# Kernel optimization log

Measured on AMD Instinct MI355X. Metric: run time of the kernel, lower is better.

The kernel has to match this reference:

```python
import jax, jax.numpy as jnp
import numpy as np

C_IN = 1024
N_HEADS = 16
C_HEAD = C_IN // N_HEADS  # 64
ROPE_BASE = 10000.0


def setup_inputs() -> dict:
    key = jax.random.key(0)
    ks = jax.random.split(key, 7)
    B, S = 2, 2048
    q = jax.random.normal(ks[0], (B, S, C_IN), dtype=jnp.float32)
    k = jax.random.normal(ks[1], (B, S, C_IN), dtype=jnp.float32)
    v = jax.random.normal(ks[2], (B, S, C_IN), dtype=jnp.float32)
    # nn.Linear weights [out, in], y = x @ W.T (no bias)
    sc = 1.0 / np.sqrt(C_IN)
    Wq = jax.random.uniform(ks[3], (C_IN, C_IN), jnp.float32, -sc, sc)
    Wk = jax.random.uniform(ks[4], (C_IN, C_IN), jnp.float32, -sc, sc)
    Wv = jax.random.uniform(ks[5], (C_IN, C_IN), jnp.float32, -sc, sc)
    Wo = jax.random.uniform(ks[6], (C_IN, C_IN), jnp.float32, -sc, sc)
    return {"q": q, "k": k, "v": v, "Wq": Wq, "Wk": Wk, "Wv": Wv, "Wo": Wo}


def _rope_tables(S, dtype):
    inv_freq = 1.0 / (ROPE_BASE ** (jnp.arange(0, C_HEAD, 2, dtype=jnp.float32) / C_HEAD))
    t = jnp.arange(S, dtype=jnp.float32)
    freqs = jnp.einsum('i,j->ij', t, inv_freq)          # [S, C_HEAD/2]
    emb = jnp.concatenate([freqs, freqs], axis=-1)      # [S, C_HEAD]
    cos = jnp.cos(emb)[None, None, :, :].astype(dtype)  # [1,1,S,D]
    sin = jnp.sin(emb)[None, None, :, :].astype(dtype)
    return cos, sin


def _rotate_half(x):
    x1, x2 = jnp.split(x, 2, axis=-1)
    return jnp.concatenate([-x2, x1], axis=-1)


def reference(q, k, v, Wq, Wk, Wv, Wo):
    B, S, _ = q.shape
    # QKV projections, reshape to [B, H, S, D]
    def proj(x, W):
        return (x @ W.T).reshape(B, -1, N_HEADS, C_HEAD).transpose(0, 2, 1, 3)
    qh, kh, vh = proj(q, Wq), proj(k, Wk), proj(v, Wv)
    # rotary embedding
    cos, sin = _rope_tables(S, qh.dtype)
    qh = qh * cos + _rotate_half(qh) * sin
    kh = kh * cos + _rotate_half(kh) * sin
    # scaled dot-product attention (no mask, dropout p=0)
    scale = 1.0 / np.sqrt(C_HEAD)
    scores = jnp.einsum('bhqd,bhkd->bhqk', qh, kh) * scale
    attn = jax.nn.softmax(scores, axis=-1)              # [B,H,S,S]
    out = jnp.einsum('bhqk,bhkd->bhqd', attn, vh)
    out = out.transpose(0, 2, 1, 3).reshape(B, S, N_HEADS * C_HEAD)
    out = out @ Wo.T
    return out, attn
```

## Files before the change

### kernel.cpp

```cpp
#include <hip/hip_runtime.h>
#include <cmath>

typedef __bf16 bhalf;
typedef __bf16 bf16x4 __attribute__((ext_vector_type(4)));
typedef __bf16 bf16x8 __attribute__((ext_vector_type(8)));
typedef float f32x4 __attribute__((ext_vector_type(4)));

#define MFMA16(a, b, c) __builtin_amdgcn_mfma_f32_16x16x32_bf16(a, b, c, 0, 0, 0)

namespace {
constexpr int Bn = 2, Sn = 2048, Cn = 1024, Hn = 16, Dn = 64;
constexpr int Zn = Bn * Hn;
constexpr int Mn = Bn * Sn;
constexpr int QTILES = 2;
}

__device__ __forceinline__ void cvt_hilo8(const float4& v0, const float4& v1,
                                          bf16x8& hi, bf16x8& lo) {
  float f[8] = {v0.x, v0.y, v0.z, v0.w, v1.x, v1.y, v1.z, v1.w};
#pragma unroll
  for (int i = 0; i < 8; ++i) {
    bhalf h = (bhalf)f[i];
    hi[i] = h;
    lo[i] = (bhalf)(f[i] - (float)h);
  }
}

template <int MODE, bool A_BF16>
__global__ __launch_bounds__(256) void proj_mfma(
    const void* __restrict__ Av, const void* __restrict__ AvLo,
    const float* __restrict__ W, float* __restrict__ out_f32,
    bhalf* __restrict__ dst_hi, bhalf* __restrict__ dst_lo) {
  __shared__ bhalf BsH[64][40];
  __shared__ bhalf BsL[64][40];
  const int tid = threadIdx.x;
  const int lane = tid & 63, w = tid >> 6;
  const int l15 = lane & 15, lg = lane >> 4;
  const int nB = blockIdx.x << 6, mB = blockIdx.y << 6;
  const int row = mB + w * 16 + l15;
  f32x4 acc[4] = {};

  const int sr = tid >> 2, sc = (tid & 3) << 3;
  for (int k0 = 0; k0 < Cn; k0 += 32) {
    {
      const float* wp = W + (size_t)(nB + sr) * Cn + k0 + sc;
      float4 w0 = *(const float4*)wp;
      float4 w1 = *(const float4*)(wp + 4);
      bf16x8 h, l;
      cvt_hilo8(w0, w1, h, l);
      *(bf16x8*)&BsH[sr][sc] = h;
      *(bf16x8*)&BsL[sr][sc] = l;
    }
    __syncthreads();
    bf16x8 aH, aL;
    if constexpr (A_BF16) {
      aH = *(const bf16x8*)((const bhalf*)Av + (size_t)row * Cn + k0 + lg * 8);
      aL = *(const bf16x8*)((const bhalf*)AvLo + (size_t)row * Cn + k0 + lg * 8);
    } else {
      const float* A = (const float*)Av;
      float4 a0 = *(const float4*)(A + (size_t)row * Cn + k0 + lg * 8);
      float4 a1 = *(const float4*)(A + (size_t)row * Cn + k0 + lg * 8 + 4);
      cvt_hilo8(a0, a1, aH, aL);
    }
#pragma unroll
    for (int j = 0; j < 4; ++j) {
      bf16x8 bH = *(const bf16x8*)&BsH[16 * j + l15][lg * 8];
      bf16x8 bL = *(const bf16x8*)&BsL[16 * j + l15][lg * 8];
      acc[j] = MFMA16(aH, bH, acc[j]);
      acc[j] = MFMA16(aH, bL, acc[j]);
      acc[j] = MFMA16(aL, bH, acc[j]);
    }
    __syncthreads();
  }

  const int mRow = mB + w * 16 + lg * 4;
  if constexpr (MODE == 0) {
#pragma unroll
    for (int j = 0; j < 4; ++j) {
      const int n = nB + 16 * j + l15;
#pragma unroll
      for (int r = 0; r < 4; ++r)
        out_f32[(size_t)(mRow + r) * Cn + n] = acc[j][r];
    }
  } else if constexpr (MODE == 1) {
    const int hh = nB >> 6;
#pragma unroll
    for (int jj = 0; jj < 2; ++jj) {
      const int d1 = 16 * jj + l15;
      const float invf = 1.0f / powf(10000.0f, (float)d1 * (1.0f / 32.0f));
#pragma unroll
      for (int r = 0; r < 4; ++r) {
        const int m = mRow + r;
        const int b = m >> 11, s = m & (Sn - 1);
        float sn, cs;
        sincosf((float)s * invf, &sn, &cs);
        const float y1 = acc[jj][r], y2 = acc[jj + 2][r];
        const float o1 = y1 * cs - y2 * sn;
        const float o2 = y2 * cs + y1 * sn;
        const size_t base = (((size_t)(b * Hn + hh)) * Sn + s) * Dn;
        bhalf h1 = (bhalf)o1, h2 = (bhalf)o2;
        dst_hi[base + d1] = h1;
        dst_lo[base + d1] = (bhalf)(o1 - (float)h1);
        dst_hi[base + d1 + 32] = h2;
        dst_lo[base + d1 + 32] = (bhalf)(o2 - (float)h2);
      }
    }
  } else {
    const int hh = nB >> 6;
#pragma unroll
    for (int j = 0; j < 4; ++j) {
      const int d = 16 * j + l15;
#pragma unroll
      for (int r = 0; r < 4; ++r) {
        const int m = mRow + r;
        const int b = m >> 11, s = m & (Sn - 1);
        dst_hi[(((size_t)(b * Hn + hh)) * Dn + d) * Sn + s] = (bhalf)acc[j][r];
      }
    }
  }
}

__device__ __forceinline__ void load_q(const bhalf* __restrict__ qhH,
                                       const bhalf* __restrict__ qhL,
                                       size_t zrow, int sBt, int l15, int lg,
                                       bf16x8 (&qH)[2][2], bf16x8 (&qL)[2][2]) {
#pragma unroll
  for (int qf = 0; qf < 2; ++qf)
#pragma unroll
    for (int sl = 0; sl < 2; ++sl) {
      const size_t off = (zrow + sBt + qf * 16 + l15) * Dn + sl * 32 + lg * 8;
      qH[qf][sl] = *(const bf16x8*)(qhH + off);
      qL[qf][sl] = *(const bf16x8*)(qhL + off);
    }
}

__global__ __launch_bounds__(256) void attn_fused(
    const bhalf* __restrict__ qhH, const bhalf* __restrict__ qhL,
    const bhalf* __restrict__ khH, const bhalf* __restrict__ khL,
    const bhalf* __restrict__ vt, float* __restrict__ attn,
    bhalf* __restrict__ ctxH, bhalf* __restrict__ ctxL) {
  __shared__ float pt[4][32][36];
  __shared__ float lsum[4][32];
  __shared__ float linv[32];

  const int tid = threadIdx.x, lane = tid & 63, w = tid >> 6;
  const int l15 = lane & 15, lg = lane >> 4;
  const int gx = blockIdx.x;
  const int z = gx & 31;
  const int gq = gx >> 5;
  const int sB0 = gq * (QTILES * 32);
  const int bb = z >> 4, hh = z & 15;
  const size_t zrow = (size_t)z * Sn;
  const size_t kRow = zrow * Dn;
  const int kw = w << 9;

  bf16x8 qHc[2][2], qLc[2][2], qHp[2][2], qLp[2][2];
  load_q(qhH, qhL, zrow, sB0, l15, lg, qHc, qLc);

  float invqB[2] = {0.f, 0.f};
  f32x4 acc[2][4];

  for (int tau = 0; tau <= QTILES; ++tau) {
    const bool hasA = (tau < QTILES), hasB = (tau > 0);
    const int sBb = sB0 + ((tau - 1) << 5);
    float sum0 = 0.f, sum1 = 0.f;
    if (hasB) {
#pragma unroll
      for (int qf = 0; qf < 2; ++qf)
#pragma unroll
        for (int g = 0; g < 4; ++g) acc[qf][g] = f32x4{0.f, 0.f, 0.f, 0.f};
    }

    for (int cc = 0; cc < 8; ++cc) {
      const int kb0 = kw + (cc << 6);
#pragma unroll
      for (int ch = 0; ch < 2; ++ch) {
        const int kbc = kb0 + (ch << 5);
#pragma unroll
        for (int t2 = 0; t2 < 2; ++t2) {
          const int kb = kbc + (t2 << 4);
          const bhalf* kp = khH + kRow + (size_t)(kb + l15) * Dn + lg * 8;
          const bhalf* kq = khL + kRow + (size_t)(kb + l15) * Dn + lg * 8;
          bf16x8 kH0 = *(const bf16x8*)kp, kH1 = *(const bf16x8*)(kp + 32);
          bf16x8 kL0 = *(const bf16x8*)kq, kL1 = *(const bf16x8*)(kq + 32);
          if (hasA) {
#pragma unroll
            for (int qf = 0; qf < 2; ++qf) {
              f32x4 cA = {}, cB = {};
              cA = MFMA16(kH0, qHc[qf][0], cA); cA = MFMA16(kH1, qHc[qf][1], cA);
              cB = MFMA16(kL0, qHc[qf][0], cB); cB = MFMA16(kL1, qHc[qf][1], cB);
              cA = MFMA16(kH0, qLc[qf][0], cA); cA = MFMA16(kH1, qLc[qf][1], cA);
              f32x4 c = cA + cB;
              float s = __expf(c[0] * 0.125f) + __expf(c[1] * 0.125f) +
                        __expf(c[2] * 0.125f) + __expf(c[3] * 0.125f);
              if (qf == 0) sum0 += s; else sum1 += s;
            }
          }
          if (hasB) {
#pragma unroll
            for (int qf = 0; qf < 2; ++qf) {
              f32x4 cA = {}, cB = {};
              cA = MFMA16(kH0, qHp[qf][0], cA); cA = MFMA16(kH1, qHp[qf][1], cA);
              cB = MFMA16(kL0, qHp[qf][0], cB); cB = MFMA16(kL1, qHp[qf][1], cB);
              cA = MFMA16(kH0, qLp[qf][0], cA); cA = MFMA16(kH1, qLp[qf][1], cA);
              f32x4 c = cA + cB;
              f32x4 p;
#pragma unroll
              for (int r = 0; r < 4; ++r)
                p[r] = __expf(c[r] * 0.125f) * invqB[qf];
              *(f32x4*)&pt[w][qf * 16 + l15][(t2 << 4) + (lg << 2)] = p;
            }
          }
        }
        if (hasB) {
          const int srow = lane >> 3, scol = (lane & 7) << 2;
#pragma unroll
          for (int s = 0; s < 4; ++s) {
            const int row = (s << 3) + srow;
            f32x4 vv = *(const f32x4*)&pt[w][row][scol];
            __builtin_nontemporal_store(
                vv, (f32x4*)(attn + (zrow + sBb + row) * Sn + kbc + scol));
          }
#pragma unroll
          for (int qf = 0; qf < 2; ++qf) {
            f32x4 pa = *(const f32x4*)&pt[w][qf * 16 + l15][lg << 3];
            f32x4 pc = *(const f32x4*)&pt[w][qf * 16 + l15][(lg << 3) + 4];
            bf16x8 pbv;
#pragma unroll
            for (int e = 0; e < 4; ++e) {
              pbv[e] = (bhalf)pa[e];
              pbv[4 + e] = (bhalf)pc[e];
            }
#pragma unroll
            for (int g = 0; g < 4; ++g) {
              const bf16x8 va = *(const bf16x8*)(
                  vt + ((size_t)z * Dn + g * 16 + l15) * Sn + kbc + lg * 8);
              acc[qf][g] = MFMA16(va, pbv, acc[qf][g]);
            }
          }
        }
      }
    }

    if (hasA) {
      sum0 += __shfl_xor(sum0, 16); sum0 += __shfl_xor(sum0, 32);
      sum1 += __shfl_xor(sum1, 16); sum1 += __shfl_xor(sum1, 32);
      if (lane < 16) {
        lsum[w][l15] = sum0;
        lsum[w][16 + l15] = sum1;
      }
    }
    __syncthreads();
    if (hasA && tid < 32)
      linv[tid] =
          1.0f / (lsum[0][tid] + lsum[1][tid] + lsum[2][tid] + lsum[3][tid]);
    if (hasB) {
      float* fb = (float*)&pt[w][0][0];
      float* fb0 = (float*)&pt[0][0][0];
      float* fb1 = (float*)&pt[1][0][0];
      float* fb2 = (float*)&pt[2][0][0];
      float* fb3 = (float*)&pt[3][0][0];
#pragma unroll
      for (int qf = 0; qf < 2; ++qf) {
#pragma unroll
        for (int g = 0; g < 4; ++g)
#pragma unroll
          for (int r = 0; r < 4; ++r)
            fb[l15 * 72 + g * 16 + lg * 4 + r] = acc[qf][g][r];
        __syncthreads();
        {
          const int qq = tid >> 4, d4 = (tid & 15) << 2;
          f32x4 rs = *(const f32x4*)&fb0[qq * 72 + d4];
          rs += *(const f32x4*)&fb1[qq * 72 + d4];
          rs += *(const f32x4*)&fb2[qq * 72 + d4];
          rs += *(const f32x4*)&fb3[qq * 72 + d4];
          const size_t off =
              ((size_t)bb * Sn + sBb + qf * 16 + qq) * Cn + hh * Dn + d4;
          bf16x4 hv, lv;
#pragma unroll
          for (int e = 0; e < 4; ++e) {
            bhalf h = (bhalf)rs[e];
            hv[e] = h;
            lv[e] = (bhalf)(rs[e] - (float)h);
          }
          *(bf16x4*)(ctxH + off) = hv;
          *(bf16x4*)(ctxL + off) = lv;
        }
        __syncthreads();
      }
    } else {
      __syncthreads();
    }
    if (hasA) {
      invqB[0] = linv[l15];
      invqB[1] = linv[16 + l15];
#pragma unroll
      for (int qf = 0; qf < 2; ++qf)
#pragma unroll
        for (int sl = 0; sl < 2; ++sl) {
          qHp[qf][sl] = qHc[qf][sl];
          qLp[qf][sl] = qLc[qf][sl];
        }
      if (tau < QTILES - 1)
        load_q(qhH, qhL, zrow, sB0 + ((tau + 1) << 5), l15, lg, qHc, qLc);
    }
  }
}

extern "C" void kernel_launch(void* const* d_in, const int* in_sizes, int n_in,
                              void* d_out, int out_size, void* d_ws, size_t ws_size,
                              hipStream_t stream) {
  const float* q = (const float*)d_in[0];
  const float* k = (const float*)d_in[1];
  const float* v = (const float*)d_in[2];
  const float* Wq = (const float*)d_in[3];
  const float* Wk = (const float*)d_in[4];
  const float* Wv = (const float*)d_in[5];
  const float* Wo = (const float*)d_in[6];

  float* out = (float*)d_out;
  float* attn = out + (size_t)Mn * Cn;
  bhalf* vt = (bhalf*)d_out;

  bhalf* qhH = (bhalf*)d_ws;
  bhalf* qhL = qhH + (size_t)Mn * Cn;
  bhalf* khH = qhL + (size_t)Mn * Cn;
  bhalf* khL = khH + (size_t)Mn * Cn;
  bhalf* ctxH = khL + (size_t)Mn * Cn;
  bhalf* ctxL = ctxH + (size_t)Mn * Cn;

  dim3 gP(Cn / 64, Mn / 64);
  proj_mfma<1, false><<<gP, 256, 0, stream>>>(q, nullptr, Wq, nullptr, qhH, qhL);
  proj_mfma<1, false><<<gP, 256, 0, stream>>>(k, nullptr, Wk, nullptr, khH, khL);
  proj_mfma<2, false><<<gP, 256, 0, stream>>>(v, nullptr, Wv, nullptr, vt, nullptr);

  attn_fused<<<Zn * (Sn / (QTILES * 32)), 256, 0, stream>>>(
      qhH, qhL, khH, khL, vt, attn, ctxH, ctxL);

  proj_mfma<0, true><<<gP, 256, 0, stream>>>(ctxH, ctxL, Wo, out, nullptr, nullptr);
}
```

Before: 461.1 us.

## Split attention keys across eight waves and process four query tiles per block

The fused attention kernel now launches 512 threads (8 waves), and each wave covers 256 keys instead of 512. The inner chunk loop drops from 64 to 32 keys per step. QTILES doubles to 4, so each block pipelines more query tiles through the two-pass softmax and amortizes the prologue and epilogue over more work. The grid halves, and cross-wave reductions of row sums and context accumulators now span 8 waves, which adds shared-memory reduction work and a larger LDS footprint per block.

After: 450.9 us. -2.2%, faster.

```diff
diff --git a/kernel.cpp b/kernel.cpp
--- a/kernel.cpp
+++ b/kernel.cpp
@@ -12,7 +12,8 @@
 constexpr int Bn = 2, Sn = 2048, Cn = 1024, Hn = 16, Dn = 64;
 constexpr int Zn = Bn * Hn;
 constexpr int Mn = Bn * Sn;
-constexpr int QTILES = 2;
+constexpr int QTILES = 4;
+constexpr int NW = 8;
 }
 
 __device__ __forceinline__ void cvt_hilo8(const float4& v0, const float4& v1,
@@ -134,13 +135,13 @@
     }
 }
 
-__global__ __launch_bounds__(256) void attn_fused(
+__global__ __launch_bounds__(512) void attn_fused(
     const bhalf* __restrict__ qhH, const bhalf* __restrict__ qhL,
     const bhalf* __restrict__ khH, const bhalf* __restrict__ khL,
     const bhalf* __restrict__ vt, float* __restrict__ attn,
     bhalf* __restrict__ ctxH, bhalf* __restrict__ ctxL) {
-  __shared__ float pt[4][32][36];
-  __shared__ float lsum[4][32];
+  __shared__ float pt[NW][32][36];
+  __shared__ float lsum[NW][32];
   __shared__ float linv[32];
 
   const int tid = threadIdx.x, lane = tid & 63, w = tid >> 6;
@@ -152,7 +153,7 @@
   const int bb = z >> 4, hh = z & 15;
   const size_t zrow = (size_t)z * Sn;
   const size_t kRow = zrow * Dn;
-  const int kw = w << 9;
+  const int kw = w << 8;
 
   bf16x8 qHc[2][2], qLc[2][2], qHp[2][2], qLp[2][2];
   load_q(qhH, qhL, zrow, sB0, l15, lg, qHc, qLc);
@@ -172,71 +173,67 @@
     }
 
     for (int cc = 0; cc < 8; ++cc) {
-      const int kb0 = kw + (cc << 6);
-#pragma unroll
-      for (int ch = 0; ch < 2; ++ch) {
-        const int kbc = kb0 + (ch << 5);
-#pragma unroll
-        for (int t2 = 0; t2 < 2; ++t2) {
-          const int kb = kbc + (t2 << 4);
-          const bhalf* kp = khH + kRow + (size_t)(kb + l15) * Dn + lg * 8;
-          const bhalf* kq = khL + kRow + (size_t)(kb + l15) * Dn + lg * 8;
-          bf16x8 kH0 = *(const bf16x8*)kp, kH1 = *(const bf16x8*)(kp + 32);
-          bf16x8 kL0 = *(const bf16x8*)kq, kL1 = *(const bf16x8*)(kq + 32);
-          if (hasA) {
-#pragma unroll
-            for (int qf = 0; qf < 2; ++qf) {
-              f32x4 cA = {}, cB = {};
-              cA = MFMA16(kH0, qHc[qf][0], cA); cA = MFMA16(kH1, qHc[qf][1], cA);
-              cB = MFMA16(kL0, qHc[qf][0], cB); cB = MFMA16(kL1, qHc[qf][1], cB);
-              cA = MFMA16(kH0, qLc[qf][0], cA); cA = MFMA16(kH1, qLc[qf][1], cA);
-              f32x4 c = cA + cB;
-              float s = __expf(c[0] * 0.125f) + __expf(c[1] * 0.125f) +
-                        __expf(c[2] * 0.125f) + __expf(c[3] * 0.125f);
-              if (qf == 0) sum0 += s; else sum1 += s;
-            }
-          }
-          if (hasB) {
-#pragma unroll
-            for (int qf = 0; qf < 2; ++qf) {
-              f32x4 cA = {}, cB = {};
-              cA = MFMA16(kH0, qHp[qf][0], cA); cA = MFMA16(kH1, qHp[qf][1], cA);
-              cB = MFMA16(kL0, qHp[qf][0], cB); cB = MFMA16(kL1, qHp[qf][1], cB);
-              cA = MFMA16(kH0, qLp[qf][0], cA); cA = MFMA16(kH1, qLp[qf][1], cA);
-              f32x4 c = cA + cB;
-              f32x4 p;
-#pragma unroll
-              for (int r = 0; r < 4; ++r)
-                p[r] = __expf(c[r] * 0.125f) * invqB[qf];
-              *(f32x4*)&pt[w][qf * 16 + l15][(t2 << 4) + (lg << 2)] = p;
-            }
+      const int kbc = kw + (cc << 5);
+#pragma unroll
+      for (int t2 = 0; t2 < 2; ++t2) {
+        const int kb = kbc + (t2 << 4);
+        const bhalf* kp = khH + kRow + (size_t)(kb + l15) * Dn + lg * 8;
+        const bhalf* kq = khL + kRow + (size_t)(kb + l15) * Dn + lg * 8;
+        bf16x8 kH0 = *(const bf16x8*)kp, kH1 = *(const bf16x8*)(kp + 32);
+        bf16x8 kL0 = *(const bf16x8*)kq, kL1 = *(const bf16x8*)(kq + 32);
+        if (hasA) {
+#pragma unroll
+          for (int qf = 0; qf < 2; ++qf) {
+            f32x4 cA = {}, cB = {};
+            cA = MFMA16(kH0, qHc[qf][0], cA); cA = MFMA16(kH1, qHc[qf][1], cA);
+            cB = MFMA16(kL0, qHc[qf][0], cB); cB = MFMA16(kL1, qHc[qf][1], cB);
+            cA = MFMA16(kH0, qLc[qf][0], cA); cA = MFMA16(kH1, qLc[qf][1], cA);
+            f32x4 c = cA + cB;
+            float s = __expf(c[0] * 0.125f) + __expf(c[1] * 0.125f) +
+                      __expf(c[2] * 0.125f) + __expf(c[3] * 0.125f);
+            if (qf == 0) sum0 += s; else sum1 += s;
           }
         }
         if (hasB) {
-          const int srow = lane >> 3, scol = (lane & 7) << 2;
-#pragma unroll
-          for (int s = 0; s < 4; ++s) {
-            const int row = (s << 3) + srow;
-            f32x4 vv = *(const f32x4*)&pt[w][row][scol];
-            __builtin_nontemporal_store(
-                vv, (f32x4*)(attn + (zrow + sBb + row) * Sn + kbc + scol));
-          }
 #pragma unroll
           for (int qf = 0; qf < 2; ++qf) {
-            f32x4 pa = *(const f32x4*)&pt[w][qf * 16 + l15][lg << 3];
-            f32x4 pc = *(const f32x4*)&pt[w][qf * 16 + l15][(lg << 3) + 4];
-            bf16x8 pbv;
-#pragma unroll
-            for (int e = 0; e < 4; ++e) {
-              pbv[e] = (bhalf)pa[e];
-              pbv[4 + e] = (bhalf)pc[e];
-            }
-#pragma unroll
-            for (int g = 0; g < 4; ++g) {
-              const bf16x8 va = *(const bf16x8*)(
-                  vt + ((size_t)z * Dn + g * 16 + l15) * Sn + kbc + lg * 8);
-              acc[qf][g] = MFMA16(va, pbv, acc[qf][g]);
-            }
+            f32x4 cA = {}, cB = {};
+            cA = MFMA16(kH0, qHp[qf][0], cA); cA = MFMA16(kH1, qHp[qf][1], cA);
+            cB = MFMA16(kL0, qHp[qf][0], cB); cB = MFMA16(kL1, qHp[qf][1], cB);
+            cA = MFMA16(kH0, qLp[qf][0], cA); cA = MFMA16(kH1, qLp[qf][1], cA);
+            f32x4 c = cA + cB;
+            f32x4 p;
+#pragma unroll
+            for (int r = 0; r < 4; ++r)
+              p[r] = __expf(c[r] * 0.125f) * invqB[qf];
+            *(f32x4*)&pt[w][qf * 16 + l15][(t2 << 4) + (lg << 2)] = p;
+          }
+        }
+      }
+      if (hasB) {
+        const int srow = lane >> 3, scol = (lane & 7) << 2;
+#pragma unroll
+        for (int s = 0; s < 4; ++s) {
+          const int row = (s << 3) + srow;
+          f32x4 vv = *(const f32x4*)&pt[w][row][scol];
+          __builtin_nontemporal_store(
+              vv, (f32x4*)(attn + (zrow + sBb + row) * Sn + kbc + scol));
+        }
+#pragma unroll
+        for (int qf = 0; qf < 2; ++qf) {
+          f32x4 pa = *(const f32x4*)&pt[w][qf * 16 + l15][lg << 3];
+          f32x4 pc = *(const f32x4*)&pt[w][qf * 16 + l15][(lg << 3) + 4];
+          bf16x8 pbv;
+#pragma unroll
+          for (int e = 0; e < 4; ++e) {
+            pbv[e] = (bhalf)pa[e];
+            pbv[4 + e] = (bhalf)pc[e];
+          }
+#pragma unroll
+          for (int g = 0; g < 4; ++g) {
+            const bf16x8 va = *(const bf16x8*)(
+                vt + ((size_t)z * Dn + g * 16 + l15) * Sn + kbc + lg * 8);
+            acc[qf][g] = MFMA16(va, pbv, acc[qf][g]);
           }
         }
       }
@@ -251,15 +248,14 @@
       }
     }
     __syncthreads();
-    if (hasA && tid < 32)
-      linv[tid] =
-          1.0f / (lsum[0][tid] + lsum[1][tid] + lsum[2][tid] + lsum[3][tid]);
+    if (hasA && tid < 32) {
+      float t = 0.f;
+#pragma unroll
+      for (int ww = 0; ww < NW; ++ww) t += lsum[ww][tid];
+      linv[tid] = 1.0f / t;
+    }
     if (hasB) {
       float* fb = (float*)&pt[w][0][0];
-      float* fb0 = (float*)&pt[0][0][0];
-      float* fb1 = (float*)&pt[1][0][0];
-      float* fb2 = (float*)&pt[2][0][0];
-      float* fb3 = (float*)&pt[3][0][0];
 #pragma unroll
       for (int qf = 0; qf < 2; ++qf) {
 #pragma unroll
@@ -268,12 +264,12 @@
           for (int r = 0; r < 4; ++r)
             fb[l15 * 72 + g * 16 + lg * 4 + r] = acc[qf][g][r];
         __syncthreads();
-        {
+        if (tid < 256) {
           const int qq = tid >> 4, d4 = (tid & 15) << 2;
-          f32x4 rs = *(const f32x4*)&fb0[qq * 72 + d4];
-          rs += *(const f32x4*)&fb1[qq * 72 + d4];
-          rs += *(const f32x4*)&fb2[qq * 72 + d4];
-          rs += *(const f32x4*)&fb3[qq * 72 + d4];
+          f32x4 rs = {0.f, 0.f, 0.f, 0.f};
+#pragma unroll
+          for (int ww = 0; ww < NW; ++ww)
+            rs += *(const f32x4*)&((float*)&pt[ww][0][0])[qq * 72 + d4];
           const size_t off =
               ((size_t)bb * Sn + sBb + qf * 16 + qq) * Cn + hh * Dn + d4;
           bf16x4 hv, lv;
@@ -334,7 +330,7 @@
   proj_mfma<1, false><<<gP, 256, 0, stream>>>(k, nullptr, Wk, nullptr, khH, khL);
   proj_mfma<2, false><<<gP, 256, 0, stream>>>(v, nullptr, Wv, nullptr, vt, nullptr);
 
-  attn_fused<<<Zn * (Sn / (QTILES * 32)), 256, 0, stream>>>(
+  attn_fused<<<Zn * (Sn / (QTILES * 32)), 512, 0, stream>>>(
       qhH, qhL, khH, khL, vt, attn, ctxH, ctxL);
 
   proj_mfma<0, true><<<gP, 256, 0, stream>>>(ctxH, ctxL, Wo, out, nullptr, nullptr);
```
